# Optimization experiments

Hardware: AMD Instinct MI355X
Metric: run time of the kernel (lower is better)

The kernel has to match this reference:

```python
import jax, jax.numpy as jnp
import numpy as np

USER_NUM = 200_000
ITEM_NUM = 100_000
N_NODES = USER_NUM + ITEM_NUM
N_EDGES = 9_600_000
LATENT_DIM = 64
N_LAYERS = 3


def setup_inputs() -> dict:
    key = jax.random.key(0)
    k1, k2, k3, k4, k5 = jax.random.split(key, 5)
    user_emb = jax.random.normal(k1, (USER_NUM, LATENT_DIM), dtype=jnp.float32)
    item_emb = jax.random.normal(k2, (ITEM_NUM, LATENT_DIM), dtype=jnp.float32)
    edge_weight = jax.random.uniform(k3, (N_EDGES,), dtype=jnp.float32)
    edge_src = jax.random.randint(k4, (N_EDGES,), 0, N_NODES, dtype=jnp.int32)
    edge_dst = jax.random.randint(k5, (N_EDGES,), 0, N_NODES, dtype=jnp.int32)
    return {
        "user_emb": user_emb,
        "item_emb": item_emb,
        "edge_weight": edge_weight,
        "edge_src": edge_src,
        "edge_dst": edge_dst,
    }


def _spmm(edge_src, edge_dst, edge_weight, x):
    # y = A @ x where A is sparse COO: A[dst, src] = w
    msg = edge_weight[:, None] * x[edge_src]          # [E, D] gather + scale
    return jax.ops.segment_sum(msg, edge_dst, num_segments=N_NODES)


def reference(user_emb, item_emb, edge_weight, edge_src, edge_dst):
    all_emb = jnp.concatenate([user_emb, item_emb], axis=0)  # [N, D]
    acc = all_emb  # running sum over layer outputs (layer 0 = raw emb)
    cur = all_emb
    for _ in range(N_LAYERS):
        cur = _spmm(edge_src, edge_dst, edge_weight, cur)
        acc = acc + cur
    light_out = acc / jnp.float32(N_LAYERS + 1)  # mean over stacked layers
    return (light_out[:USER_NUM], light_out[USER_NUM:])
```

## Files before the change

kernel.cpp:

```cpp
#include <hip/hip_runtime.h>
#include <hip/hip_fp16.h>

#define USER_NUM 200000
#define ITEM_NUM 100000
#define N_NODES  300000
#define N_EDGES  9600000
#define D        64
#define NELEM    ((long long)N_NODES * D)
#define NELEM4   (NELEM / 4)

#define CAP 96

#define SRC_MASK 0x7FFFFu
#define W_SCALE  (1.0f / 8191.0f)

#define BIN_NODES 1024
#define BIN_SHIFT 10
#define NBINS     ((N_NODES + BIN_NODES - 1) / BIN_NODES)
#define EPB       7168
#define NBLK_A    ((N_EDGES + EPB - 1) / EPB)
#define BPG       ((NBLK_A + 15) / 16)

__global__ void init_kernel(const float4* __restrict__ user_emb,
                            const float4* __restrict__ item_emb,
                            float4* __restrict__ out,
                            ushort4* __restrict__ cur) {
    long long i = (long long)blockIdx.x * blockDim.x + threadIdx.x;
    if (i >= NELEM4) return;
    const long long user4 = (long long)USER_NUM * D / 4;
    float4 v = (i < user4) ? user_emb[i] : item_emb[i - user4];
    out[i] = v;
    __half h0 = __float2half_rn(v.x), h1 = __float2half_rn(v.y);
    __half h2 = __float2half_rn(v.z), h3 = __float2half_rn(v.w);
    cur[i] = make_ushort4(*(unsigned short*)&h0, *(unsigned short*)&h1,
                          *(unsigned short*)&h2, *(unsigned short*)&h3);
}

__global__ __launch_bounds__(512) void binA_kernel(
        const int*   __restrict__ src,
        const int*   __restrict__ dst,
        const float* __restrict__ w,
        unsigned long long* __restrict__ seg,
        unsigned*           __restrict__ blk_info) {
    __shared__ unsigned long long stage[EPB];
    __shared__ int hist[NBINS];
    __shared__ int off[NBINS];
    const int tid = threadIdx.x;
    const long long e0 = (long long)blockIdx.x * EPB;
    long long rem = (long long)N_EDGES - e0;
    const int nE = (int)(rem < EPB ? rem : EPB);

    for (int i = tid; i < NBINS; i += 512) hist[i] = 0;
    __syncthreads();

    for (int k = tid * 4; k < nE; k += 512 * 4) {
        int4 d4 = *(const int4*)(dst + e0 + k);
        atomicAdd(&hist[d4.x >> BIN_SHIFT], 1);
        atomicAdd(&hist[d4.y >> BIN_SHIFT], 1);
        atomicAdd(&hist[d4.z >> BIN_SHIFT], 1);
        atomicAdd(&hist[d4.w >> BIN_SHIFT], 1);
    }
    __syncthreads();

    if (tid < NBINS) off[tid] = hist[tid];
    __syncthreads();
    for (int s = 1; s < NBINS; s <<= 1) {
        int v = 0;
        if (tid < NBINS && tid >= s) v = off[tid - s];
        __syncthreads();
        if (tid < NBINS && tid >= s) off[tid] += v;
        __syncthreads();
    }
    if (tid < NBINS) {
        int excl = off[tid] - hist[tid];
        off[tid] = excl;
        blk_info[(long long)tid * NBLK_A + blockIdx.x] =
            ((unsigned)excl << 16) | (unsigned)hist[tid];
    }
    __syncthreads();

    for (int k = tid * 4; k < nE; k += 512 * 4) {
        int4   s4 = *(const int4*)(src + e0 + k);
        int4   d4 = *(const int4*)(dst + e0 + k);
        float4 w4 = *(const float4*)(w + e0 + k);
#define DO_EDGE(S, DD, W) { \
        unsigned q = (unsigned)((W) * 8191.0f + 0.5f); \
        int bin = (DD) >> BIN_SHIFT; \
        int pos = atomicAdd(&off[bin], 1); \
        stage[pos] = ((unsigned long long)(unsigned)((DD) & (BIN_NODES - 1)) << 32) \
                   | ((q << 19) | (unsigned)(S)); }
        DO_EDGE(s4.x, d4.x, w4.x)
        DO_EDGE(s4.y, d4.y, w4.y)
        DO_EDGE(s4.z, d4.z, w4.z)
        DO_EDGE(s4.w, d4.w, w4.w)
#undef DO_EDGE
    }
    __syncthreads();

    for (int k = tid; k < nE; k += 512)
        seg[e0 + k] = stage[k];
}

__global__ __launch_bounds__(512) void binB_kernel(
        const unsigned*           __restrict__ blk_info,
        const unsigned long long* __restrict__ seg,
        int*      __restrict__ deg,
        unsigned* __restrict__ slots) {
    __shared__ int dl[BIN_NODES];
    __shared__ unsigned info[NBLK_A];
    const int bin = blockIdx.x;
    const int tid = threadIdx.x;
    dl[tid] = 0; dl[tid + 512] = 0;
    for (int i = tid; i < NBLK_A; i += 512)
        info[i] = blk_info[(long long)bin * NBLK_A + i];
    __syncthreads();

    const int node0 = bin << BIN_SHIFT;
    const int grp = tid >> 5;
    const int gl  = tid & 31;
    int b1 = grp * BPG + BPG;
    if (b1 > NBLK_A) b1 = NBLK_A;
    for (int blk = grp * BPG; blk < b1; ++blk) {
        unsigned inf = info[blk];
        int cnt = (int)(inf & 0xFFFFu);
        long long base = (long long)blk * EPB + (inf >> 16);
        for (int j = gl; j < cnt; j += 32) {
            unsigned long long v = seg[base + j];
            int l = (int)(v >> 32);
            int p = atomicAdd(&dl[l], 1);
            if (p < CAP) slots[(long long)(node0 + l) * CAP + p] = (unsigned)v;
        }
    }
    __syncthreads();

    int node = node0 + tid;
    if (node < N_NODES) deg[node] = dl[tid];
    node += 512;
    if (tid + 512 < BIN_NODES && node < N_NODES) deg[node] = dl[tid + 512];
}

template <bool LAST>
__global__ void spmm_gather(const int*      __restrict__ deg,
                            const unsigned* __restrict__ slots,
                            const __half2*  __restrict__ cur,
                            __half2*        __restrict__ next,
                            float2*         __restrict__ out) {
    long long t = (long long)blockIdx.x * blockDim.x + threadIdx.x;
    int wave = (int)(t >> 6);
    int lane = (int)(t & 63);
    int half = lane >> 5;
    int col  = lane & 31;
    int node = wave * 2 + half;
    if (node >= N_NODES) return;
    int n = deg[node];
    if (n > CAP) n = CAP;
    const unsigned* sl = slots + (long long)node * CAP;
    float accx = 0.f, accy = 0.f;
    int i = 0;
    for (; i + 3 < n; i += 4) {
        unsigned e0 = sl[i + 0];
        unsigned e1 = sl[i + 1];
        unsigned e2 = sl[i + 2];
        unsigned e3 = sl[i + 3];
        __half2 x0 = cur[(long long)(e0 & SRC_MASK) * 32 + col];
        __half2 x1 = cur[(long long)(e1 & SRC_MASK) * 32 + col];
        __half2 x2 = cur[(long long)(e2 & SRC_MASK) * 32 + col];
        __half2 x3 = cur[(long long)(e3 & SRC_MASK) * 32 + col];
        float w0 = (float)(e0 >> 19) * W_SCALE;
        float w1 = (float)(e1 >> 19) * W_SCALE;
        float w2 = (float)(e2 >> 19) * W_SCALE;
        float w3 = (float)(e3 >> 19) * W_SCALE;
        float2 f0 = __half22float2(x0);
        float2 f1 = __half22float2(x1);
        float2 f2 = __half22float2(x2);
        float2 f3 = __half22float2(x3);
        accx = fmaf(w0, f0.x, accx); accy = fmaf(w0, f0.y, accy);
        accx = fmaf(w1, f1.x, accx); accy = fmaf(w1, f1.y, accy);
        accx = fmaf(w2, f2.x, accx); accy = fmaf(w2, f2.y, accy);
        accx = fmaf(w3, f3.x, accx); accy = fmaf(w3, f3.y, accy);
    }
    for (; i < n; ++i) {
        unsigned e0 = sl[i];
        __half2 x0 = cur[(long long)(e0 & SRC_MASK) * 32 + col];
        float w0 = (float)(e0 >> 19) * W_SCALE;
        float2 f0 = __half22float2(x0);
        accx = fmaf(w0, f0.x, accx); accy = fmaf(w0, f0.y, accy);
    }
    long long oi = (long long)node * 32 + col;
    if (!LAST) {
        __half2 h; h.x = __float2half_rn(accx); h.y = __float2half_rn(accy);
        next[oi] = h;
    }
    float2 o = out[oi];
    o.x += accx; o.y += accy;
    if (LAST) { o.x *= 0.25f; o.y *= 0.25f; }
    out[oi] = o;
}

extern "C" void kernel_launch(void* const* d_in, const int* in_sizes, int n_in,
                              void* d_out, int out_size, void* d_ws, size_t ws_size,
                              hipStream_t stream) {
    const float* user_emb = (const float*)d_in[0];
    const float* item_emb = (const float*)d_in[1];
    const float* ew       = (const float*)d_in[2];
    const int*   es       = (const int*)d_in[3];
    const int*   ed       = (const int*)d_in[4];
    float* out = (float*)d_out;

    unsigned* slots = (unsigned*)d_ws;
    int*      deg   = (int*)((char*)d_ws + (long long)N_NODES * CAP * 4);
    __half*   buf0  = (__half*)(deg + N_NODES);
    __half*   buf1  = buf0 + NELEM;
    unsigned long long* seg = (unsigned long long*)buf0;
    unsigned* blk_info = (unsigned*)(seg + (long long)NBLK_A * EPB);

    const int B = 256;
    const long long node_waves  = (N_NODES + 1) / 2;
    const long long node_blocks = (node_waves * 64 + B - 1) / B;
    const long long init_blocks = (NELEM4 + B - 1) / B;

    binA_kernel<<<dim3((unsigned)NBLK_A), dim3(512), 0, stream>>>(
        es, ed, ew, seg, blk_info);
    binB_kernel<<<dim3((unsigned)NBINS), dim3(512), 0, stream>>>(
        blk_info, seg, deg, slots);

    init_kernel<<<dim3((unsigned)init_blocks), dim3(B), 0, stream>>>(
        (const float4*)user_emb, (const float4*)item_emb,
        (float4*)out, (ushort4*)buf0);

    spmm_gather<false><<<dim3((unsigned)node_blocks), dim3(B), 0, stream>>>(
        deg, slots, (const __half2*)buf0, (__half2*)buf1, (float2*)out);
    spmm_gather<false><<<dim3((unsigned)node_blocks), dim3(B), 0, stream>>>(
        deg, slots, (const __half2*)buf1, (__half2*)buf0, (float2*)out);
    spmm_gather<true><<<dim3((unsigned)node_blocks), dim3(B), 0, stream>>>(
        deg, slots, (const __half2*)buf0, (__half2*)buf1, (float2*)out);
}
```

Baseline: 967.1 us.

## Defer fp32 output accumulation to last layer and widen gather unroll

The fp32 output is no longer written at init or read and written in every layer. Each layer's fp16 result is now kept in its own buffer (a third buffer is added), and the final layer sums the fp16 copies of layers 0 to 2 with its own result, then scales the sum. The gather loop also loads slot entries as uint4, unrolls 8 edges per iteration and splits the work over two accumulator pairs to expose more memory-level parallelism. This removes several full passes over the fp32 output, at the cost of more workspace and of summing layer 0 from the fp16 copy instead of the original fp32 embeddings, which slightly lowers accuracy.

```diff
diff --git a/kernel.cpp b/kernel.cpp
--- a/kernel.cpp
+++ b/kernel.cpp
@@ -23,13 +23,11 @@
 
 __global__ void init_kernel(const float4* __restrict__ user_emb,
                             const float4* __restrict__ item_emb,
-                            float4* __restrict__ out,
                             ushort4* __restrict__ cur) {
     long long i = (long long)blockIdx.x * blockDim.x + threadIdx.x;
     if (i >= NELEM4) return;
     const long long user4 = (long long)USER_NUM * D / 4;
     float4 v = (i < user4) ? user_emb[i] : item_emb[i - user4];
-    out[i] = v;
     __half h0 = __float2half_rn(v.x), h1 = __float2half_rn(v.y);
     __half h2 = __float2half_rn(v.z), h3 = __float2half_rn(v.w);
     cur[i] = make_ushort4(*(unsigned short*)&h0, *(unsigned short*)&h1,
@@ -144,6 +142,8 @@
                             const unsigned* __restrict__ slots,
                             const __half2*  __restrict__ cur,
                             __half2*        __restrict__ next,
+                            const __half2*  __restrict__ x0b,
+                            const __half2*  __restrict__ x1b,
                             float2*         __restrict__ out) {
     long long t = (long long)blockIdx.x * blockDim.x + threadIdx.x;
     int wave = (int)(t >> 6);
@@ -156,28 +156,62 @@
     if (n > CAP) n = CAP;
     const unsigned* sl = slots + (long long)node * CAP;
     float accx = 0.f, accy = 0.f;
+    float bccx = 0.f, bccy = 0.f;
     int i = 0;
+    for (; i + 7 < n; i += 8) {
+        uint4 ea = *(const uint4*)(sl + i);
+        uint4 eb = *(const uint4*)(sl + i + 4);
+        __half2 x0 = cur[(long long)(ea.x & SRC_MASK) * 32 + col];
+        __half2 x1 = cur[(long long)(ea.y & SRC_MASK) * 32 + col];
+        __half2 x2 = cur[(long long)(ea.z & SRC_MASK) * 32 + col];
+        __half2 x3 = cur[(long long)(ea.w & SRC_MASK) * 32 + col];
+        __half2 x4 = cur[(long long)(eb.x & SRC_MASK) * 32 + col];
+        __half2 x5 = cur[(long long)(eb.y & SRC_MASK) * 32 + col];
+        __half2 x6 = cur[(long long)(eb.z & SRC_MASK) * 32 + col];
+        __half2 x7 = cur[(long long)(eb.w & SRC_MASK) * 32 + col];
+        float w0 = (float)(ea.x >> 19) * W_SCALE;
+        float w1 = (float)(ea.y >> 19) * W_SCALE;
+        float w2 = (float)(ea.z >> 19) * W_SCALE;
+        float w3 = (float)(ea.w >> 19) * W_SCALE;
+        float w4 = (float)(eb.x >> 19) * W_SCALE;
+        float w5 = (float)(eb.y >> 19) * W_SCALE;
+        float w6 = (float)(eb.z >> 19) * W_SCALE;
+        float w7 = (float)(eb.w >> 19) * W_SCALE;
+        float2 f0 = __half22float2(x0);
+        float2 f1 = __half22float2(x1);
+        float2 f2 = __half22float2(x2);
+        float2 f3 = __half22float2(x3);
+        float2 f4 = __half22float2(x4);
+        float2 f5 = __half22float2(x5);
+        float2 f6 = __half22float2(x6);
+        float2 f7 = __half22float2(x7);
+        accx = fmaf(w0, f0.x, accx); accy = fmaf(w0, f0.y, accy);
+        bccx = fmaf(w1, f1.x, bccx); bccy = fmaf(w1, f1.y, bccy);
+        accx = fmaf(w2, f2.x, accx); accy = fmaf(w2, f2.y, accy);
+        bccx = fmaf(w3, f3.x, bccx); bccy = fmaf(w3, f3.y, bccy);
+        accx = fmaf(w4, f4.x, accx); accy = fmaf(w4, f4.y, accy);
+        bccx = fmaf(w5, f5.x, bccx); bccy = fmaf(w5, f5.y, bccy);
+        accx = fmaf(w6, f6.x, accx); accy = fmaf(w6, f6.y, accy);
+        bccx = fmaf(w7, f7.x, bccx); bccy = fmaf(w7, f7.y, bccy);
+    }
     for (; i + 3 < n; i += 4) {
-        unsigned e0 = sl[i + 0];
-        unsigned e1 = sl[i + 1];
-        unsigned e2 = sl[i + 2];
-        unsigned e3 = sl[i + 3];
-        __half2 x0 = cur[(long long)(e0 & SRC_MASK) * 32 + col];
-        __half2 x1 = cur[(long long)(e1 & SRC_MASK) * 32 + col];
-        __half2 x2 = cur[(long long)(e2 & SRC_MASK) * 32 + col];
-        __half2 x3 = cur[(long long)(e3 & SRC_MASK) * 32 + col];
-        float w0 = (float)(e0 >> 19) * W_SCALE;
-        float w1 = (float)(e1 >> 19) * W_SCALE;
-        float w2 = (float)(e2 >> 19) * W_SCALE;
-        float w3 = (float)(e3 >> 19) * W_SCALE;
+        uint4 ea = *(const uint4*)(sl + i);
+        __half2 x0 = cur[(long long)(ea.x & SRC_MASK) * 32 + col];
+        __half2 x1 = cur[(long long)(ea.y & SRC_MASK) * 32 + col];
+        __half2 x2 = cur[(long long)(ea.z & SRC_MASK) * 32 + col];
+        __half2 x3 = cur[(long long)(ea.w & SRC_MASK) * 32 + col];
+        float w0 = (float)(ea.x >> 19) * W_SCALE;
+        float w1 = (float)(ea.y >> 19) * W_SCALE;
+        float w2 = (float)(ea.z >> 19) * W_SCALE;
+        float w3 = (float)(ea.w >> 19) * W_SCALE;
         float2 f0 = __half22float2(x0);
         float2 f1 = __half22float2(x1);
         float2 f2 = __half22float2(x2);
         float2 f3 = __half22float2(x3);
         accx = fmaf(w0, f0.x, accx); accy = fmaf(w0, f0.y, accy);
-        accx = fmaf(w1, f1.x, accx); accy = fmaf(w1, f1.y, accy);
+        bccx = fmaf(w1, f1.x, bccx); bccy = fmaf(w1, f1.y, bccy);
         accx = fmaf(w2, f2.x, accx); accy = fmaf(w2, f2.y, accy);
-        accx = fmaf(w3, f3.x, accx); accy = fmaf(w3, f3.y, accy);
+        bccx = fmaf(w3, f3.x, bccx); bccy = fmaf(w3, f3.y, bccy);
     }
     for (; i < n; ++i) {
         unsigned e0 = sl[i];
@@ -186,15 +220,20 @@
         float2 f0 = __half22float2(x0);
         accx = fmaf(w0, f0.x, accx); accy = fmaf(w0, f0.y, accy);
     }
+    accx += bccx; accy += bccy;
     long long oi = (long long)node * 32 + col;
     if (!LAST) {
         __half2 h; h.x = __float2half_rn(accx); h.y = __float2half_rn(accy);
         next[oi] = h;
-    }
-    float2 o = out[oi];
-    o.x += accx; o.y += accy;
-    if (LAST) { o.x *= 0.25f; o.y *= 0.25f; }
-    out[oi] = o;
+    } else {
+        float2 f0 = __half22float2(x0b[oi]);
+        float2 f1 = __half22float2(x1b[oi]);
+        float2 f2 = __half22float2(cur[oi]);
+        float2 o;
+        o.x = (f0.x + f1.x + f2.x + accx) * 0.25f;
+        o.y = (f0.y + f1.y + f2.y + accy) * 0.25f;
+        out[oi] = o;
+    }
 }
 
 extern "C" void kernel_launch(void* const* d_in, const int* in_sizes, int n_in,
@@ -208,11 +247,12 @@
     float* out = (float*)d_out;
 
     unsigned* slots = (unsigned*)d_ws;
-    int*      deg   = (int*)((char*)d_ws + (long long)N_NODES * CAP * 4);
+    int*      deg   = (int*)(slots + (long long)N_NODES * CAP);
     __half*   buf0  = (__half*)(deg + N_NODES);
     __half*   buf1  = buf0 + NELEM;
+    __half*   buf2  = buf1 + NELEM;
+    unsigned* blk_info = (unsigned*)(buf2 + NELEM);
     unsigned long long* seg = (unsigned long long*)buf0;
-    unsigned* blk_info = (unsigned*)(seg + (long long)NBLK_A * EPB);
 
     const int B = 256;
     const long long node_waves  = (N_NODES + 1) / 2;
@@ -225,13 +265,15 @@
         blk_info, seg, deg, slots);
 
     init_kernel<<<dim3((unsigned)init_blocks), dim3(B), 0, stream>>>(
-        (const float4*)user_emb, (const float4*)item_emb,
-        (float4*)out, (ushort4*)buf0);
+        (const float4*)user_emb, (const float4*)item_emb, (ushort4*)buf0);
 
     spmm_gather<false><<<dim3((unsigned)node_blocks), dim3(B), 0, stream>>>(
-        deg, slots, (const __half2*)buf0, (__half2*)buf1, (float2*)out);
+        deg, slots, (const __half2*)buf0, (__half2*)buf1,
+        nullptr, nullptr, nullptr);
     spmm_gather<false><<<dim3((unsigned)node_blocks), dim3(B), 0, stream>>>(
-        deg, slots, (const __half2*)buf1, (__half2*)buf0, (float2*)out);
+        deg, slots, (const __half2*)buf1, (__half2*)buf2,
+        nullptr, nullptr, nullptr);
     spmm_gather<true><<<dim3((unsigned)node_blocks), dim3(B), 0, stream>>>(
-        deg, slots, (const __half2*)buf0, (__half2*)buf1, (float2*)out);
-}
+        deg, slots, (const __half2*)buf2, nullptr,
+        (const __half2*)buf0, (const __half2*)buf1, (float2*)out);
+}
```

Result: faster. 866.5 us (-10.4%).

## Defer fp32 accumulation to final layer using fp16 layer buffers and wider gathers

Applied to the files above, without the earlier changes.

Stops writing the fp32 output in init and in every layer. Each layer's fp16 output is kept in its own buffer (a third buffer is added), and the last layer sums the raw embedding plus all three layers once. Each gather thread now loads 8 bytes (4 halves) with 16 lanes per node, slot indices are read as uint4 vectors, and the weight scale is applied once after the loop. This cuts fp32 read-modify-write traffic and per-edge multiplies. In exchange, the layer-0 and intermediate terms of the final sum now come from fp16 copies, which lowers precision, and the workspace layout changes with blk_info moved after buf2.

```diff
diff --git a/kernel.cpp b/kernel.cpp
--- a/kernel.cpp
+++ b/kernel.cpp
@@ -23,13 +23,11 @@
 
 __global__ void init_kernel(const float4* __restrict__ user_emb,
                             const float4* __restrict__ item_emb,
-                            float4* __restrict__ out,
                             ushort4* __restrict__ cur) {
     long long i = (long long)blockIdx.x * blockDim.x + threadIdx.x;
     if (i >= NELEM4) return;
     const long long user4 = (long long)USER_NUM * D / 4;
     float4 v = (i < user4) ? user_emb[i] : item_emb[i - user4];
-    out[i] = v;
     __half h0 = __float2half_rn(v.x), h1 = __float2half_rn(v.y);
     __half h2 = __float2half_rn(v.z), h3 = __float2half_rn(v.w);
     cur[i] = make_ushort4(*(unsigned short*)&h0, *(unsigned short*)&h1,
@@ -142,59 +140,72 @@
 template <bool LAST>
 __global__ void spmm_gather(const int*      __restrict__ deg,
                             const unsigned* __restrict__ slots,
-                            const __half2*  __restrict__ cur,
-                            __half2*        __restrict__ next,
-                            float2*         __restrict__ out) {
+                            const uint2*    __restrict__ cur,
+                            uint2*          __restrict__ next,
+                            const uint2*    __restrict__ x0b,
+                            const uint2*    __restrict__ x1b,
+                            float4*         __restrict__ out) {
     long long t = (long long)blockIdx.x * blockDim.x + threadIdx.x;
     int wave = (int)(t >> 6);
     int lane = (int)(t & 63);
-    int half = lane >> 5;
-    int col  = lane & 31;
-    int node = wave * 2 + half;
+    int g    = lane >> 4;
+    int c    = lane & 15;
+    int node = wave * 4 + g;
     if (node >= N_NODES) return;
     int n = deg[node];
     if (n > CAP) n = CAP;
     const unsigned* sl = slots + (long long)node * CAP;
-    float accx = 0.f, accy = 0.f;
+    float a0 = 0.f, a1 = 0.f, a2 = 0.f, a3 = 0.f;
+
+#define GATHER(E) { \
+        unsigned e_ = (E); \
+        uint2 hv = cur[((long long)(e_ & SRC_MASK) << 4) + c]; \
+        float q_ = (float)(e_ >> 19); \
+        __half2 h01 = *reinterpret_cast<const __half2*>(&hv.x); \
+        __half2 h23 = *reinterpret_cast<const __half2*>(&hv.y); \
+        a0 = fmaf(__low2float(h01),  q_, a0); \
+        a1 = fmaf(__high2float(h01), q_, a1); \
+        a2 = fmaf(__low2float(h23),  q_, a2); \
+        a3 = fmaf(__high2float(h23), q_, a3); }
+
     int i = 0;
+    for (; i + 7 < n; i += 8) {
+        uint4 ea = *(const uint4*)(sl + i);
+        uint4 eb = *(const uint4*)(sl + i + 4);
+        GATHER(ea.x) GATHER(ea.y) GATHER(ea.z) GATHER(ea.w)
+        GATHER(eb.x) GATHER(eb.y) GATHER(eb.z) GATHER(eb.w)
+    }
     for (; i + 3 < n; i += 4) {
-        unsigned e0 = sl[i + 0];
-        unsigned e1 = sl[i + 1];
-        unsigned e2 = sl[i + 2];
-        unsigned e3 = sl[i + 3];
-        __half2 x0 = cur[(long long)(e0 & SRC_MASK) * 32 + col];
-        __half2 x1 = cur[(long long)(e1 & SRC_MASK) * 32 + col];
-        __half2 x2 = cur[(long long)(e2 & SRC_MASK) * 32 + col];
-        __half2 x3 = cur[(long long)(e3 & SRC_MASK) * 32 + col];
-        float w0 = (float)(e0 >> 19) * W_SCALE;
-        float w1 = (float)(e1 >> 19) * W_SCALE;
-        float w2 = (float)(e2 >> 19) * W_SCALE;
-        float w3 = (float)(e3 >> 19) * W_SCALE;
-        float2 f0 = __half22float2(x0);
-        float2 f1 = __half22float2(x1);
-        float2 f2 = __half22float2(x2);
-        float2 f3 = __half22float2(x3);
-        accx = fmaf(w0, f0.x, accx); accy = fmaf(w0, f0.y, accy);
-        accx = fmaf(w1, f1.x, accx); accy = fmaf(w1, f1.y, accy);
-        accx = fmaf(w2, f2.x, accx); accy = fmaf(w2, f2.y, accy);
-        accx = fmaf(w3, f3.x, accx); accy = fmaf(w3, f3.y, accy);
+        uint4 ea = *(const uint4*)(sl + i);
+        GATHER(ea.x) GATHER(ea.y) GATHER(ea.z) GATHER(ea.w)
     }
     for (; i < n; ++i) {
-        unsigned e0 = sl[i];
-        __half2 x0 = cur[(long long)(e0 & SRC_MASK) * 32 + col];
-        float w0 = (float)(e0 >> 19) * W_SCALE;
-        float2 f0 = __half22float2(x0);
-        accx = fmaf(w0, f0.x, accx); accy = fmaf(w0, f0.y, accy);
-    }
-    long long oi = (long long)node * 32 + col;
+        GATHER(sl[i])
+    }
+#undef GATHER
+
+    a0 *= W_SCALE; a1 *= W_SCALE; a2 *= W_SCALE; a3 *= W_SCALE;
+    long long oi = (long long)node * 16 + c;
     if (!LAST) {
-        __half2 h; h.x = __float2half_rn(accx); h.y = __float2half_rn(accy);
-        next[oi] = h;
-    }
-    float2 o = out[oi];
-    o.x += accx; o.y += accy;
-    if (LAST) { o.x *= 0.25f; o.y *= 0.25f; }
-    out[oi] = o;
+        __half2 p01 = __float22half2_rn(make_float2(a0, a1));
+        __half2 p23 = __float22half2_rn(make_float2(a2, a3));
+        next[oi] = make_uint2(*reinterpret_cast<unsigned*>(&p01),
+                              *reinterpret_cast<unsigned*>(&p23));
+    } else {
+        uint2 v0 = x0b[oi], v1 = x1b[oi], v2 = cur[oi];
+        __half2 u01 = *reinterpret_cast<const __half2*>(&v0.x);
+        __half2 u23 = *reinterpret_cast<const __half2*>(&v0.y);
+        __half2 w01 = *reinterpret_cast<const __half2*>(&v1.x);
+        __half2 w23 = *reinterpret_cast<const __half2*>(&v1.y);
+        __half2 z01 = *reinterpret_cast<const __half2*>(&v2.x);
+        __half2 z23 = *reinterpret_cast<const __half2*>(&v2.y);
+        float4 o;
+        o.x = (__low2float(u01)  + __low2float(w01)  + __low2float(z01)  + a0) * 0.25f;
+        o.y = (__high2float(u01) + __high2float(w01) + __high2float(z01) + a1) * 0.25f;
+        o.z = (__low2float(u23)  + __low2float(w23)  + __low2float(z23)  + a2) * 0.25f;
+        o.w = (__high2float(u23) + __high2float(w23) + __high2float(z23) + a3) * 0.25f;
+        out[oi] = o;
+    }
 }
 
 extern "C" void kernel_launch(void* const* d_in, const int* in_sizes, int n_in,
@@ -208,14 +219,15 @@
     float* out = (float*)d_out;
 
     unsigned* slots = (unsigned*)d_ws;
-    int*      deg   = (int*)((char*)d_ws + (long long)N_NODES * CAP * 4);
+    int*      deg   = (int*)(slots + (long long)N_NODES * CAP);
     __half*   buf0  = (__half*)(deg + N_NODES);
     __half*   buf1  = buf0 + NELEM;
+    __half*   buf2  = buf1 + NELEM;
+    unsigned* blk_info = (unsigned*)(buf2 + NELEM);
     unsigned long long* seg = (unsigned long long*)buf0;
-    unsigned* blk_info = (unsigned*)(seg + (long long)NBLK_A * EPB);
 
     const int B = 256;
-    const long long node_waves  = (N_NODES + 1) / 2;
+    const long long node_waves  = (N_NODES + 3) / 4;
     const long long node_blocks = (node_waves * 64 + B - 1) / B;
     const long long init_blocks = (NELEM4 + B - 1) / B;
 
@@ -225,13 +237,15 @@
         blk_info, seg, deg, slots);
 
     init_kernel<<<dim3((unsigned)init_blocks), dim3(B), 0, stream>>>(
-        (const float4*)user_emb, (const float4*)item_emb,
-        (float4*)out, (ushort4*)buf0);
+        (const float4*)user_emb, (const float4*)item_emb, (ushort4*)buf0);
 
     spmm_gather<false><<<dim3((unsigned)node_blocks), dim3(B), 0, stream>>>(
-        deg, slots, (const __half2*)buf0, (__half2*)buf1, (float2*)out);
+        deg, slots, (const uint2*)buf0, (uint2*)buf1,
+        nullptr, nullptr, nullptr);
     spmm_gather<false><<<dim3((unsigned)node_blocks), dim3(B), 0, stream>>>(
-        deg, slots, (const __half2*)buf1, (__half2*)buf0, (float2*)out);
+        deg, slots, (const uint2*)buf1, (uint2*)buf2,
+        nullptr, nullptr, nullptr);
     spmm_gather<true><<<dim3((unsigned)node_blocks), dim3(B), 0, stream>>>(
-        deg, slots, (const __half2*)buf0, (__half2*)buf1, (float2*)out);
-}
+        deg, slots, (const uint2*)buf2, nullptr,
+        (const uint2*)buf0, (const uint2*)buf1, (float4*)out);
+}
```

Measured after the change: 869.3 us. 10.1% less time.
